# Kernel tuning notes

Hardware: AMD Instinct MI355X
Metric: run time of the kernel (lower is better)

The kernel has to match this reference:

```python
import jax, jax.numpy as jnp
import numpy as np

B = 512        # batch size
NCLASS = 128   # number of classes == embedding dim (per module docstring)
K = 8          # topk hard mining
MARGIN = 1.0
P = 1.0 / NCLASS  # default p = 1/nclass


def _pairwise_distances(x):
    # Euclidean distance matrix, with the zero-distance sqrt-safety trick
    dot = x @ x.T                      # (B, B)
    sq = jnp.diag(dot)                 # (B,)
    d = sq[None, :] - 2.0 * dot + sq[:, None]
    d = jnp.maximum(d, 0.0)
    zmask = (d == 0.0).astype(x.dtype)
    return (1.0 - zmask) * jnp.sqrt(d + zmask * 1e-16)


def _topk_rows_mask(valid):
    # torch .topk(k, dim=0, largest=True) + scatter_(0, idx, True):
    # per column, mark the k rows with the largest values.
    _, idx = jax.lax.top_k(valid.T, K)                 # (B, K): row indices per column
    mT = jnp.zeros((B, B), dtype=bool).at[jnp.arange(B)[:, None], idx].set(True)
    return mT.T                                        # back to (row, col) layout


def _forward(x, target):
    d = _pairwise_distances(x)                         # (B, B)
    sim = target[None, :] == target[:, None]           # (B, B) same-class mask

    # hard positives: largest same-class distances per column
    hard_pos = _topk_rows_mask(jnp.where(sim, d, -jnp.inf)) & sim
    # hard negatives: smallest different-class distances per column
    hard_neg = _topk_rows_mask(-jnp.where(sim, jnp.inf, d)) & (~sim)

    # minor-class anchors: class count < int(p * batch)
    boundary = int(P * B)
    cnt = jnp.zeros((NCLASS,), dtype=jnp.int32).at[target].add(1)
    anchors = cnt[target] < boundary                   # (B,)

    eye = jnp.eye(B, dtype=bool)
    mask_ap = (~eye) & anchors[:, None] & hard_pos     # (B, B)
    mask_an = anchors[:, None] & hard_neg              # (B, B)

    # O(B^3) triplet tensor
    t = d[:, :, None] - d[:, None, :] + MARGIN         # (B, B, B)
    m = mask_ap[:, :, None] & mask_an[:, None, :]
    t = jnp.maximum(m.astype(x.dtype) * t, 0.0)
    num_pos = jnp.sum(t > 1e-7).astype(x.dtype)
    return jnp.sum(t) / (num_pos + 1e-7)


def setup_inputs() -> dict:
    key = jax.random.key(0)
    k1, k2 = jax.random.split(key)
    x = jax.random.normal(k1, (B, NCLASS), dtype=jnp.float32)
    target = jax.random.randint(k2, (B,), 0, NCLASS)
    return {"x": x, "target": target}


def reference(x, target):
    return _forward(x, target)
```

## Files before the change

### kernel.cpp

```cpp
#include <hip/hip_runtime.h>
#include <math.h>

#define BB 512
#define DD 128
#define KK 8
#define BOUNDARY 4


__global__ __launch_bounds__(512, 4) void fused_kernel(
    const float* __restrict__ x, const int* __restrict__ tgt,
    float* __restrict__ partS, int* __restrict__ partC)
{
    __shared__ float4 xi4[DD / 4];
    __shared__ float s_vn[BB];
    __shared__ float s_sq[BB];
    __shared__ int   s_tgt[BB];
    __shared__ int   s_cnt[128];
    __shared__ int   s_sel[KK];
    __shared__ int   s_pr[16], s_pj[16];
    __shared__ int   s_np;

    int k = blockIdx.x;
    int t = threadIdx.x;
    if (t < DD / 4) xi4[t] = ((const float4*)(x + k * DD))[t];
    if (t < 128) s_cnt[t] = 0;
    if (t == 0) s_np = 0;
    s_tgt[t] = tgt[t];
    __syncthreads();
    int tk = s_tgt[k];

    float q0 = 0.f, q1 = 0.f, q2 = 0.f, q3 = 0.f;
    for (int c = 0; c < DD / 4; ++c) {
        float4 a = xi4[c];
        q0 += a.x * a.x; q1 += a.y * a.y; q2 += a.z * a.z; q3 += a.w * a.w;
    }
    float sqk = (q0 + q1) + (q2 + q3);

    {
        int g = t >> 3, sub = t & 7;
        for (int pass = 0; pass < 8; ++pass) {
            int r = pass * 64 + g;
            const float4* xr = (const float4*)(x + r * DD);
            float d0, d1, d2, d3, s0, s1, s2, s3;
            {
                float4 a = xi4[sub],      b = xr[sub];
                d0 = a.x*b.x + a.y*b.y + a.z*b.z + a.w*b.w;
                s0 = b.x*b.x + b.y*b.y + b.z*b.z + b.w*b.w;
            }
            {
                float4 a = xi4[sub + 8],  b = xr[sub + 8];
                d1 = a.x*b.x + a.y*b.y + a.z*b.z + a.w*b.w;
                s1 = b.x*b.x + b.y*b.y + b.z*b.z + b.w*b.w;
            }
            {
                float4 a = xi4[sub + 16], b = xr[sub + 16];
                d2 = a.x*b.x + a.y*b.y + a.z*b.z + a.w*b.w;
                s2 = b.x*b.x + b.y*b.y + b.z*b.z + b.w*b.w;
            }
            {
                float4 a = xi4[sub + 24], b = xr[sub + 24];
                d3 = a.x*b.x + a.y*b.y + a.z*b.z + a.w*b.w;
                s3 = b.x*b.x + b.y*b.y + b.z*b.z + b.w*b.w;
            }
            float dot = (d0 + d1) + (d2 + d3);
            float sq  = (s0 + s1) + (s2 + s3);
            for (int off = 4; off > 0; off >>= 1) {
                dot += __shfl_down(dot, off, 8);
                sq  += __shfl_down(sq,  off, 8);
            }
            if (sub == 0) {
                float dsq = fmaxf((sqk + sq) - 2.f * dot, 0.f);
                float dv = (dsq == 0.f) ? 0.f : sqrtf(dsq);
                s_sq[r] = sq;
                s_vn[r] = (s_tgt[r] == tk) ? -INFINITY : -dv;
            }
        }
    }
    __syncthreads();

    int wave = t >> 6, lane = t & 63;
    if (wave == 0) {
        float v[8];
        for (int q = 0; q < 8; ++q) v[q] = s_vn[q * 64 + lane];
        for (int pass = 0; pass < KK; ++pass) {
            float bv = -INFINITY; int bq = -1;
            for (int q = 0; q < 8; ++q)
                if (v[q] > bv) { bv = v[q]; bq = q; }
            int bi = (bq >= 0) ? (bq * 64 + lane) : (1 << 30);
            for (int off = 32; off > 0; off >>= 1) {
                float ov = __shfl_down(bv, off);
                int   oi = __shfl_down(bi, off);
                if (ov > bv || (ov == bv && oi < bi)) { bv = ov; bi = oi; }
            }
            bv = __shfl(bv, 0); bi = __shfl(bi, 0);
            if (lane == 0) s_sel[pass] = (bv == -INFINITY) ? -1 : bi;
            if ((bi & 63) == lane) v[bi >> 6] = -INFINITY;
        }
    } else if (wave == 1) {
        for (int q = 0; q < 8; ++q) atomicAdd(&s_cnt[s_tgt[q * 64 + lane]], 1);
    }
    __syncthreads();

    {
        int r = s_sel[wave];
        if (r >= 0) {
            int tr = s_tgt[r];
            if (s_cnt[tr] < BOUNDARY) {
                for (int j = lane; j < BB; j += 64)
                    if (j != r && s_tgt[j] == tr) {
                        int idx = atomicAdd(&s_np, 1);
                        s_pr[idx] = r; s_pj[idx] = j;
                    }
            }
        }
    }
    __syncthreads();

    float s = 0.f; int c = 0;
    if (t < s_np) {
        int r = s_pr[t], j = s_pj[t];
        const float4* xr = (const float4*)(x + r * DD);
        const float4* xj = (const float4*)(x + j * DD);
        float d0 = 0.f, d1 = 0.f, d2 = 0.f, d3 = 0.f;
        for (int cc = 0; cc < DD / 4; ++cc) {
            float4 a = xr[cc], b = xj[cc];
            d0 += a.x * b.x; d1 += a.y * b.y; d2 += a.z * b.z; d3 += a.w * b.w;
        }
        float dot = (d0 + d1) + (d2 + d3);
        float dsq = fmaxf((s_sq[r] + s_sq[j]) - 2.f * dot, 0.f);
        float dpos = (dsq == 0.f) ? 0.f : sqrtf(dsq);
        float tv = dpos + s_vn[r] + 1.0f;
        if (tv > 0.f) { s = tv; c = (tv > 1e-7f) ? 1 : 0; }
    }
    if (wave == 0) {
        for (int off = 32; off > 0; off >>= 1) {
            s += __shfl_down(s, off);
            c += __shfl_down(c, off);
        }
        if (lane == 0) { partS[k] = s; partC[k] = c; }
    }
}

__global__ __launch_bounds__(64) void fin_kernel(
    const float* __restrict__ partS, const int* __restrict__ partC,
    float* __restrict__ out)
{
    int lane = threadIdx.x;
    const float4* pS = (const float4*)partS;
    const int4*   pC = (const int4*)partC;
    float4 a = pS[lane], b = pS[lane + 64];
    int4   u = pC[lane], v = pC[lane + 64];
    float S = ((a.x + a.y) + (a.z + a.w)) + ((b.x + b.y) + (b.z + b.w));
    int   C = ((u.x + u.y) + (u.z + u.w)) + ((v.x + v.y) + (v.z + v.w));
    for (int off = 32; off > 0; off >>= 1) {
        S += __shfl_down(S, off);
        C += __shfl_down(C, off);
    }
    if (lane == 0) out[0] = S / ((float)C + 1e-7f);
}

extern "C" void kernel_launch(void* const* d_in, const int* in_sizes, int n_in,
                              void* d_out, int out_size, void* d_ws, size_t ws_size,
                              hipStream_t stream) {
    const float* x   = (const float*)d_in[0];
    const int*   tgt = (const int*)d_in[1];
    float* out = (float*)d_out;

    char* ws = (char*)d_ws;
    float* partS = (float*)(ws + 0);
    int*   partC = (int*)(ws + 2048);

    fused_kernel<<<BB, 512, 0, stream>>>(x, tgt, partS, partC);
    fin_kernel<<<1, 64, 0, stream>>>(partS, partC, out);
}
```

Before: 72.02 us.

## Split into tiled distance-matrix kernel plus per-column selection kernel

Adds a tiled 32x32 shared-memory kernel that computes the full pairwise distance matrix into workspace, followed by a lightweight 64-thread-per-column kernel that does top-k negative selection, class counting and positive-distance lookup from that matrix. This replaces the fused kernel, in which every block re-read all of x to build one column and recomputed positive dot products. The cost is an extra launch and a 1 MB write and read of the matrix. The fused kernel remains as a fallback when the workspace is too small, and its register-indexed pop is rewritten as an unrolled predicated loop.

```diff
diff --git a/kernel.cpp b/kernel.cpp
--- a/kernel.cpp
+++ b/kernel.cpp
@@ -6,6 +6,159 @@
 #define KK 8
 #define BOUNDARY 4
 
+
+__global__ __launch_bounds__(256) void dist_kernel(
+    const float* __restrict__ x, float* __restrict__ Dm)
+{
+    __shared__ float4 As[32 * 33];
+    __shared__ float4 Bs[32 * 33];
+    __shared__ float  sqA[32], sqB[32];
+
+    const int t  = threadIdx.x;
+    const int r0 = blockIdx.y * 32;
+    const int c0 = blockIdx.x * 32;
+
+    const float4* xa = (const float4*)(x + r0 * DD);
+    const float4* xb = (const float4*)(x + c0 * DD);
+#pragma unroll
+    for (int i = 0; i < 4; ++i) {
+        int f = t + 256 * i;
+        int row = f >> 5, col = f & 31;
+        As[row * 33 + col] = xa[f];
+        Bs[row * 33 + col] = xb[f];
+    }
+    __syncthreads();
+
+    if (t < 64) {
+        const float4* P = (t < 32) ? As : Bs;
+        int row = t & 31;
+        float s0 = 0.f, s1 = 0.f, s2 = 0.f, s3 = 0.f;
+#pragma unroll 8
+        for (int k = 0; k < 32; ++k) {
+            float4 a = P[row * 33 + k];
+            s0 += a.x * a.x; s1 += a.y * a.y; s2 += a.z * a.z; s3 += a.w * a.w;
+        }
+        float s = (s0 + s1) + (s2 + s3);
+        if (t < 32) sqA[row] = s; else sqB[row] = s;
+    }
+    __syncthreads();
+
+    const int cl = t & 31;
+    const int rg = (t >> 5) * 4;
+    float4 acc0 = {0,0,0,0}, acc1 = {0,0,0,0}, acc2 = {0,0,0,0}, acc3 = {0,0,0,0};
+#pragma unroll 8
+    for (int k = 0; k < 32; ++k) {
+        float4 b  = Bs[cl * 33 + k];
+        float4 a0 = As[(rg + 0) * 33 + k];
+        float4 a1 = As[(rg + 1) * 33 + k];
+        float4 a2 = As[(rg + 2) * 33 + k];
+        float4 a3 = As[(rg + 3) * 33 + k];
+        acc0.x += a0.x * b.x; acc0.y += a0.y * b.y; acc0.z += a0.z * b.z; acc0.w += a0.w * b.w;
+        acc1.x += a1.x * b.x; acc1.y += a1.y * b.y; acc1.z += a1.z * b.z; acc1.w += a1.w * b.w;
+        acc2.x += a2.x * b.x; acc2.y += a2.y * b.y; acc2.z += a2.z * b.z; acc2.w += a2.w * b.w;
+        acc3.x += a3.x * b.x; acc3.y += a3.y * b.y; acc3.z += a3.z * b.z; acc3.w += a3.w * b.w;
+    }
+    float d0 = (acc0.x + acc0.y) + (acc0.z + acc0.w);
+    float d1 = (acc1.x + acc1.y) + (acc1.z + acc1.w);
+    float d2 = (acc2.x + acc2.y) + (acc2.z + acc2.w);
+    float d3 = (acc3.x + acc3.y) + (acc3.z + acc3.w);
+    float sb = sqB[cl];
+    float q0 = fmaxf((sqA[rg + 0] + sb) - 2.f * d0, 0.f);
+    float q1 = fmaxf((sqA[rg + 1] + sb) - 2.f * d1, 0.f);
+    float q2 = fmaxf((sqA[rg + 2] + sb) - 2.f * d2, 0.f);
+    float q3 = fmaxf((sqA[rg + 3] + sb) - 2.f * d3, 0.f);
+    float4 o;
+    o.x = (q0 == 0.f) ? 0.f : sqrtf(q0);
+    o.y = (q1 == 0.f) ? 0.f : sqrtf(q1);
+    o.z = (q2 == 0.f) ? 0.f : sqrtf(q2);
+    o.w = (q3 == 0.f) ? 0.f : sqrtf(q3);
+    *(float4*)(Dm + (c0 + cl) * BB + (r0 + rg)) = o;
+}
+
+__global__ __launch_bounds__(64) void select_kernel(
+    const float* __restrict__ Dm, const int* __restrict__ tgt,
+    float* __restrict__ partS, int* __restrict__ partC)
+{
+    __shared__ int   s_tgt[BB];
+    __shared__ int   s_cnt[128];
+    __shared__ int   s_sel[KK];
+    __shared__ float s_selv[KK];
+    __shared__ int   s_pr[16], s_pj[16];
+    __shared__ float s_pv[16];
+    __shared__ int   s_np;
+
+    const int k = blockIdx.x;
+    const int lane = threadIdx.x;
+
+    s_cnt[lane] = 0; s_cnt[lane + 64] = 0;
+    if (lane == 0) s_np = 0;
+#pragma unroll
+    for (int q = 0; q < 8; ++q) s_tgt[q * 64 + lane] = tgt[q * 64 + lane];
+    __syncthreads();
+
+    const int tk = s_tgt[k];
+#pragma unroll
+    for (int q = 0; q < 8; ++q) atomicAdd(&s_cnt[s_tgt[q * 64 + lane]], 1);
+
+    const float* col = Dm + k * BB;
+    float v[8];
+#pragma unroll
+    for (int q = 0; q < 8; ++q) {
+        int r = q * 64 + lane;
+        v[q] = (s_tgt[r] == tk) ? -INFINITY : -col[r];
+    }
+
+    for (int pass = 0; pass < KK; ++pass) {
+        float bv = -INFINITY; int bq = -1;
+#pragma unroll
+        for (int q = 0; q < 8; ++q)
+            if (v[q] > bv) { bv = v[q]; bq = q; }
+        int bi = (bq >= 0) ? (bq * 64 + lane) : (1 << 30);
+        for (int off = 32; off > 0; off >>= 1) {
+            float ov = __shfl_down(bv, off);
+            int   oi = __shfl_down(bi, off);
+            if (ov > bv || (ov == bv && oi < bi)) { bv = ov; bi = oi; }
+        }
+        bv = __shfl(bv, 0); bi = __shfl(bi, 0);
+        if (lane == 0) { s_sel[pass] = (bv == -INFINITY) ? -1 : bi; s_selv[pass] = bv; }
+        const int  popq = bi >> 6;
+        const bool mine = ((bi & 63) == lane);
+#pragma unroll
+        for (int q = 0; q < 8; ++q)
+            if (mine && q == popq) v[q] = -INFINITY;
+    }
+    __syncthreads();
+
+    for (int s = 0; s < KK; ++s) {
+        int r = s_sel[s];
+        if (r < 0) continue;
+        int tr = s_tgt[r];
+        if (s_cnt[tr] >= BOUNDARY) continue;
+        float vn = s_selv[s];
+#pragma unroll
+        for (int q = 0; q < 8; ++q) {
+            int j = q * 64 + lane;
+            if (j != r && s_tgt[j] == tr) {
+                int idx = atomicAdd(&s_np, 1);
+                s_pr[idx] = r; s_pj[idx] = j; s_pv[idx] = vn;
+            }
+        }
+    }
+    __syncthreads();
+
+    float s = 0.f; int c = 0;
+    if (lane < s_np) {
+        int r = s_pr[lane], j = s_pj[lane];
+        float dpos = Dm[j * BB + r];
+        float tv = dpos + s_pv[lane] + 1.0f;
+        if (tv > 0.f) { s = tv; c = (tv > 1e-7f) ? 1 : 0; }
+    }
+    for (int off = 32; off > 0; off >>= 1) {
+        s += __shfl_down(s, off);
+        c += __shfl_down(c, off);
+    }
+    if (lane == 0) { partS[k] = s; partC[k] = c; }
+}
 
 __global__ __launch_bounds__(512, 4) void fused_kernel(
     const float* __restrict__ x, const int* __restrict__ tgt,
@@ -84,6 +237,7 @@
         for (int q = 0; q < 8; ++q) v[q] = s_vn[q * 64 + lane];
         for (int pass = 0; pass < KK; ++pass) {
             float bv = -INFINITY; int bq = -1;
+#pragma unroll
             for (int q = 0; q < 8; ++q)
                 if (v[q] > bv) { bv = v[q]; bq = q; }
             int bi = (bq >= 0) ? (bq * 64 + lane) : (1 << 30);
@@ -94,7 +248,11 @@
             }
             bv = __shfl(bv, 0); bi = __shfl(bi, 0);
             if (lane == 0) s_sel[pass] = (bv == -INFINITY) ? -1 : bi;
-            if ((bi & 63) == lane) v[bi >> 6] = -INFINITY;
+            const int  popq = bi >> 6;
+            const bool mine = ((bi & 63) == lane);
+#pragma unroll
+            for (int q = 0; q < 8; ++q)
+                if (mine && q == popq) v[q] = -INFINITY;
         }
     } else if (wave == 1) {
         for (int q = 0; q < 8; ++q) atomicAdd(&s_cnt[s_tgt[q * 64 + lane]], 1);
@@ -169,7 +327,13 @@
     char* ws = (char*)d_ws;
     float* partS = (float*)(ws + 0);
     int*   partC = (int*)(ws + 2048);
-
-    fused_kernel<<<BB, 512, 0, stream>>>(x, tgt, partS, partC);
+    float* Dm    = (float*)(ws + 4096);
+
+    if (ws_size >= 4096 + (size_t)BB * BB * sizeof(float)) {
+        dist_kernel<<<dim3(16, 16), 256, 0, stream>>>(x, Dm);
+        select_kernel<<<BB, 64, 0, stream>>>(Dm, tgt, partS, partC);
+    } else {
+        fused_kernel<<<BB, 512, 0, stream>>>(x, tgt, partS, partC);
+    }
     fin_kernel<<<1, 64, 0, stream>>>(partS, partC, out);
 }
```

New measurement: 74.78 us. 3.8% more time.
